# Kernel tuning notes

Hardware: AMD Instinct MI355X
Metric: run time of the kernel (lower is better)

Reference implementation:

```python
import jax, jax.numpy as jnp
import numpy as np

KS = 3

def setup_inputs() -> dict:
    key = jax.random.key(0)
    k1, k2, k3 = jax.random.split(key, 3)
    x = jax.random.normal(k1, (4, 4, 256, 36, 36), dtype=jnp.float32)
    target_filter = jax.random.normal(k2, (1024, 256, KS, KS), dtype=jnp.float32) * 0.05
    # per-sample (b=num_img*num_sq=16) positive scale factors; p_n is scaled by ks/offset
    offset = 1.0 + 2.0 * jax.random.uniform(k3, (16, 2), dtype=jnp.float32)
    return {"x": x, "target_filter": target_filter, "offset": offset}


def _deform_sample(xf, offset, ks):
    # xf: [b, ct, h, w] -> bilinearly sampled x_offset: [b, ct, h, w, N], N = ks*ks
    b, ct, h, w = xf.shape
    N = ks * ks
    pad = ks // 2
    xp = jnp.pad(xf, ((0, 0), (0, 0), (pad, pad), (pad, pad)))  # zero padding as in torch
    Hp, Wp = h + 2 * pad, w + 2 * pad
    dt = xf.dtype
    # kernel grid offsets p_n (row-major: n = i*ks + j, i=row/x, j=col/y)
    r = jnp.arange(-(ks - 1) // 2, (ks - 1) // 2 + 1, dtype=dt)
    pnx, pny = jnp.meshgrid(r, r, indexing='ij')
    pnx = pnx.reshape(N)
    pny = pny.reshape(N)
    # base positions p_0 (in padded coordinates)
    p0x = jnp.arange(pad, h + pad, dtype=dt)
    p0y = jnp.arange(pad, w + pad, dtype=dt)
    # per-sample scales ks / offset
    sx = (ks / offset[:, 0])[:, None, None, None]  # [b,1,1,1]
    sy = (ks / offset[:, 1])[:, None, None, None]
    # sampling positions, kept factored: px [b,h,1,N], py [b,1,w,N]
    px = p0x[None, :, None, None] + pnx[None, None, None, :] * sx
    py = p0y[None, None, :, None] + pny[None, None, None, :] * sy
    pxc = jnp.clip(px, 0.0, Hp - 1)
    pyc = jnp.clip(py, 0.0, Wp - 1)
    # integer corners (detached/int in torch as well)
    qltx = jnp.clip(jnp.floor(px), 0.0, Hp - 1)
    qrbx = jnp.clip(jnp.floor(px) + 1.0, 0.0, Hp - 1)
    qlty = jnp.clip(jnp.floor(py), 0.0, Wp - 1)
    qrby = jnp.clip(jnp.floor(py) + 1.0, 0.0, Wp - 1)
    qltx_i = jax.lax.stop_gradient(qltx).astype(jnp.int32)
    qrbx_i = jax.lax.stop_gradient(qrbx).astype(jnp.int32)
    qlty_i = jax.lax.stop_gradient(qlty).astype(jnp.int32)
    qrby_i = jax.lax.stop_gradient(qrby).astype(jnp.int32)
    # bilinear weights, factored per-axis (broadcast b,h,1,N x b,1,w,N)
    gx_l = 1.0 + (jax.lax.stop_gradient(qltx) - pxc)
    gx_r = 1.0 - (jax.lax.stop_gradient(qrbx) - pxc)
    gy_l = 1.0 + (jax.lax.stop_gradient(qlty) - pyc)
    gy_r = 1.0 - (jax.lax.stop_gradient(qrby) - pyc)
    xflat = xp.reshape(b, ct, Hp * Wp)

    def gather(qx, qy):
        idx = jnp.broadcast_to(qx * Wp + qy, (b, h, w, N)).reshape(b, h * w * N)
        g = jax.vmap(lambda xb, ib: jnp.take(xb, ib, axis=1))(xflat, idx)
        return g.reshape(b, ct, h, w, N)

    x_off = ((gx_l * gy_l)[:, None] * gather(qltx_i, qlty_i)
             + (gx_r * gy_r)[:, None] * gather(qrbx_i, qrby_i)
             + (gx_l * gy_r)[:, None] * gather(qltx_i, qrby_i)
             + (gx_r * gy_l)[:, None] * gather(qrbx_i, qlty_i))
    return x_off  # [b, ct, h, w, N]


def reference(x, target_filter, offset):
    # feat_group=False path of DeformConv2d.forward
    ks = target_filter.shape[-1]
    num_img, num_sq, ct, h, w = x.shape
    xf = x.reshape(num_img * num_sq, ct, h, w)
    x_off = _deform_sample(xf, offset, ks)  # [b, ct, h, w, ks*ks]
    out_ch = target_filter.shape[0]
    outg = out_ch // num_sq
    # grouped conv2d with stride=ks over the im2col-style layout == direct einsum
    f = target_filter.reshape(num_sq, outg, ct, ks, ks)
    xo = x_off.reshape(num_img, num_sq, ct, h, w, ks, ks)
    out = jnp.einsum('gocij,mgcyxij->mgoyx', f, xo)
    return out.reshape(num_img, out_ch, h, w)
```

## Files before the change

### kernel.cpp

```cpp
#include <hip/hip_runtime.h>
#include <hip/hip_bf16.h>


#define HH 36
#define WW 36
#define CT 256
#define NB 16
#define KK 2304
#define NP 1296
#define OCH 1024
#define OUTG 256

typedef __attribute__((ext_vector_type(8))) short short8;
typedef __attribute__((ext_vector_type(4))) float f32x4;
typedef __attribute__((ext_vector_type(4))) unsigned short us4;
typedef __attribute__((ext_vector_type(4))) unsigned uint4v;

__device__ __forceinline__ unsigned short f2bf(float v) {
    unsigned u = __float_as_uint(v);
    u += 0x7fffu + ((u >> 16) & 1u);
    return (unsigned short)(u >> 16);
}
__device__ __forceinline__ unsigned pk2bf(float lo, float hi) {
    __hip_bfloat162 h = __float22bfloat162_rn(float2{lo, hi});
    return *reinterpret_cast<unsigned*>(&h);
}

__global__ __launch_bounds__(256) void cvt_filter(const float* __restrict__ f,
                                                  unsigned short* __restrict__ w) {
    const int o = blockIdx.x;
    const float* fo = f + (size_t)o * KK;
    unsigned short* wo = w + (size_t)o * KK;
    for (int k4 = threadIdx.x * 4; k4 < KK; k4 += 1024) {
        int n = k4 >> 8;
        int c = k4 & 255;
        us4 v;
#pragma unroll
        for (int cc = 0; cc < 4; ++cc) v[cc] = f2bf(fo[(c + cc) * 9 + n]);
        *reinterpret_cast<us4*>(wo + k4) = v;
    }
}

__global__ __launch_bounds__(256) void sample_kernel(const float* __restrict__ x,
                                                     const float* __restrict__ off,
                                                     unsigned short* __restrict__ xt) {
    const int wid = (blockIdx.x & 7) * 144 + (blockIdx.x >> 3);
    const int b = wid / 72;
    const int rem = wid - b * 72;
    const int y = rem >> 1;
    const int half = rem & 1;
    const int tid = threadIdx.x;
    const float sx = 3.0f / off[2 * b + 0];
    const float sy = 3.0f / off[2 * b + 1];

    int qxl[3], qxr[3]; float gxl[3], gxr[3];
    bool lok[3], rok[3];
#pragma unroll
    for (int i = 0; i < 3; ++i) {
        float px = (float)(y + 1) + (float)(i - 1) * sx;
        float pc = fminf(fmaxf(px, 0.f), 37.f);
        float fl = floorf(px);
        float ql = fminf(fmaxf(fl, 0.f), 37.f);
        float qr = fminf(fmaxf(fl + 1.f, 0.f), 37.f);
        qxl[i] = (int)ql; qxr[i] = (int)qr;
        gxl[i] = 1.f + (ql - pc);
        gxr[i] = 1.f - (qr - pc);
        lok[i] = (qxl[i] >= 1 && qxl[i] <= 36);
        rok[i] = (qxr[i] >= 1 && qxr[i] <= 36);
    }

    __shared__ int   s_qyl[HH * 3], s_qyr[HH * 3];
    __shared__ float s_gyl[HH * 3], s_gyr[HH * 3];
    if (tid < HH * 3) {
        int xx = tid / 3, j = tid % 3;
        float py = (float)(xx + 1) + (float)(j - 1) * sy;
        float pc = fminf(fmaxf(py, 0.f), 37.f);
        float fl = floorf(py);
        float ql = fminf(fmaxf(fl, 0.f), 37.f);
        float qr = fminf(fmaxf(fl + 1.f, 0.f), 37.f);
        s_qyl[tid] = (int)ql; s_qyr[tid] = (int)qr;
        s_gyl[tid] = 1.f + (ql - pc);
        s_gyr[tid] = 1.f - (qr - pc);
    }

    __shared__ float xr[3 * 38 * 64];

    for (int chunk = 0; chunk < 2; ++chunk) {
        const int c0 = half * 128 + chunk * 64;
        __syncthreads();

        for (int t = tid; t < 384; t += 256) {
            int i = t / 128, r3 = t & 127;
            int col = (r3 & 64) ? 37 : 0, c = r3 & 63;
            xr[(i * 38 + col) * 64 + c] = 0.f;
        }

        const float* xb = x + (size_t)(b * CT + c0) * NP;
        for (int t = tid; t < 3 * 64 * 9; t += 256) {
            const int i = t / 576;
            const int r2 = t - i * 576;
            const int c = r2 / 9;
            const int cq = r2 - c * 9;
            const int colb = 1 + cq * 4;
            const float* xc = xb + c * NP;
            float4 vl = make_float4(0.f, 0.f, 0.f, 0.f);
            float4 vr = vl;
            if (lok[i]) vl = *(const float4*)(xc + (qxl[i] - 1) * WW + colb - 1);
            if (rok[i]) vr = *(const float4*)(xc + (qxr[i] - 1) * WW + colb - 1);
            float* dst = &xr[(i * 38 + colb) * 64 + c];
            dst[0]   = gxl[i] * vl.x + gxr[i] * vr.x;
            dst[64]  = gxl[i] * vl.y + gxr[i] * vr.y;
            dst[128] = gxl[i] * vl.z + gxr[i] * vr.z;
            dst[192] = gxl[i] * vl.w + gxr[i] * vr.w;
        }
        __syncthreads();

        for (int t = tid; t < 36 * 8; t += 256) {
            const int xi = t >> 3;
            const int c8 = t & 7;
            unsigned short* op = xt + ((size_t)b * NP + y * WW + xi) * KK + c0 + c8 * 8;
#pragma unroll
            for (int n = 0; n < 9; ++n) {
                const int i = n / 3, j = n - i * 3;
                const int tq = xi * 3 + j;
                const float gl = s_gyl[tq], gr = s_gyr[tq];
                const float* L = &xr[(i * 38 + s_qyl[tq]) * 64 + c8 * 8];
                const float* R = &xr[(i * 38 + s_qyr[tq]) * 64 + c8 * 8];
                f32x4 L0 = *(const f32x4*)L, L1 = *(const f32x4*)(L + 4);
                f32x4 R0 = *(const f32x4*)R, R1 = *(const f32x4*)(R + 4);
                uint4v w;
                w[0] = pk2bf(gl * L0[0] + gr * R0[0], gl * L0[1] + gr * R0[1]);
                w[1] = pk2bf(gl * L0[2] + gr * R0[2], gl * L0[3] + gr * R0[3]);
                w[2] = pk2bf(gl * L1[0] + gr * R1[0], gl * L1[1] + gr * R1[1]);
                w[3] = pk2bf(gl * L1[2] + gr * R1[2], gl * L1[3] + gr * R1[3]);
                *reinterpret_cast<uint4v*>(op + n * 256) = w;
            }
        }
    }
}

__global__ __launch_bounds__(256) void gemm_kernel(const unsigned short* __restrict__ wbf,
                                                   const unsigned short* __restrict__ xt,
                                                   float* __restrict__ out) {
    const int wid = (blockIdx.x & 7) * 84 + (blockIdx.x >> 3);
    const int b = wid / 42;
    const int rem = wid - b * 42;
    const int mt = rem / 21;
    const int nt = rem - mt * 21;
    const int m0 = mt * 128;
    const int p0 = nt * 64;
    const int g = b & 3;
    const int mimg = b >> 2;

    const unsigned short* Ab = wbf + (size_t)(g * OUTG + m0) * KK;
    const unsigned short* Bb = xt + (size_t)b * NP * KK;

    __shared__ __align__(16) unsigned short As[2][128 * 64];
    __shared__ __align__(16) unsigned short Bs[2][64 * 64];

    const int tid = threadIdx.x;
    const int wave = tid >> 6, lane = tid & 63;
    const int wr = wave >> 1, wc = wave & 1;
    const int l8 = lane >> 3;
    const int sgrp = (lane & 7) ^ l8;

    f32x4 acc[4][2] = {};

#define STAGE(BUF, KT) do {                                                       \
    const int k0_ = (KT) * 64;                                                    \
    _Pragma("unroll")                                                             \
    for (int ii = 0; ii < 4; ++ii) {                                              \
        const int inst = wave * 4 + ii;                                           \
        const int row = inst * 8 + l8;                                            \
        const unsigned short* srcA = Ab + (size_t)row * KK + k0_ + sgrp * 8;      \
        __builtin_amdgcn_global_load_lds(                                         \
            (const __attribute__((address_space(1))) void*)srcA,                  \
            (__attribute__((address_space(3))) void*)&As[BUF][inst * 512], 16, 0, 0); \
    }                                                                             \
    _Pragma("unroll")                                                             \
    for (int ii = 0; ii < 2; ++ii) {                                              \
        const int inst = wave * 2 + ii;                                           \
        const int row = inst * 8 + l8;                                            \
        int prow = p0 + row;                                                      \
        prow = prow < NP ? prow : NP - 1;                                         \
        const unsigned short* srcB = Bb + (size_t)prow * KK + k0_ + sgrp * 8;     \
        __builtin_amdgcn_global_load_lds(                                         \
            (const __attribute__((address_space(1))) void*)srcB,                  \
            (__attribute__((address_space(3))) void*)&Bs[BUF][inst * 512], 16, 0, 0); \
    }                                                                             \
} while (0)

#define COMPUTE(BUF) do {                                                         \
    _Pragma("unroll")                                                             \
    for (int kk = 0; kk < 2; ++kk) {                                              \
        short8 a[4], bfr[2];                                                      \
        const int g8 = (((kk * 4) + (lane >> 4)) ^ (lane & 7)) << 3;              \
        const int rA = wr * 64 + (lane & 15);                                     \
        const int rB = wc * 32 + (lane & 15);                                     \
        _Pragma("unroll")                                                         \
        for (int m = 0; m < 4; ++m)                                               \
            a[m] = *(const short8*)&As[BUF][(rA + m * 16) * 64 + g8];             \
        _Pragma("unroll")                                                         \
        for (int n = 0; n < 2; ++n)                                               \
            bfr[n] = *(const short8*)&Bs[BUF][(rB + n * 16) * 64 + g8];           \
        _Pragma("unroll")                                                         \
        for (int m = 0; m < 4; ++m)                                               \
            _Pragma("unroll")                                                     \
            for (int n = 0; n < 2; ++n)                                           \
                acc[m][n] = __builtin_amdgcn_mfma_f32_16x16x32_bf16(              \
                    a[m], bfr[n], acc[m][n], 0, 0, 0);                            \
    }                                                                             \
} while (0)

    STAGE(0, 0);

#pragma unroll 1
    for (int kt = 0; kt < 35; ++kt) {
        STAGE((kt + 1) & 1, kt + 1);
        asm volatile("s_waitcnt vmcnt(6)" ::: "memory");
        __builtin_amdgcn_sched_barrier(0);
        __builtin_amdgcn_s_barrier();
        COMPUTE(kt & 1);
        __builtin_amdgcn_s_barrier();
    }
    asm volatile("s_waitcnt vmcnt(0)" ::: "memory");
    __builtin_amdgcn_sched_barrier(0);
    __builtin_amdgcn_s_barrier();
    COMPUTE(35 & 1);

#undef STAGE
#undef COMPUTE

    float* ob = out + ((size_t)mimg * OCH + g * OUTG) * NP;
    const int o0 = m0 + wr * 64 + ((lane >> 4) << 2);
    const int pc = p0 + wc * 32 + (lane & 15);
#pragma unroll
    for (int n = 0; n < 2; ++n) {
        int p = pc + n * 16;
        if (p >= NP) continue;
#pragma unroll
        for (int m = 0; m < 4; ++m) {
#pragma unroll
            for (int r = 0; r < 4; ++r)
                ob[(size_t)(o0 + m * 16 + r) * NP + p] = acc[m][n][r];
        }
    }
}

extern "C" void kernel_launch(void* const* d_in, const int* in_sizes, int n_in,
                              void* d_out, int out_size, void* d_ws, size_t ws_size,
                              hipStream_t stream) {
    const float* x   = (const float*)d_in[0];
    const float* tf  = (const float*)d_in[1];
    const float* off = (const float*)d_in[2];
    float* out = (float*)d_out;

    unsigned short* xt  = (unsigned short*)d_ws;
    unsigned short* wbf = xt + (size_t)NB * NP * KK;

    hipLaunchKernelGGL(cvt_filter, dim3(OCH), dim3(256), 0, stream, tf, wbf);
    hipLaunchKernelGGL(sample_kernel, dim3(NB * HH * 2), dim3(256), 0, stream, x, off, xt);
    hipLaunchKernelGGL(gemm_kernel, dim3(672), dim3(256), 0, stream, wbf, xt, out);
}
```

Baseline: 72.45 us.

## Load GEMM A-operand directly into registers, bypassing LDS staging

```diff
diff --git a/kernel.cpp b/kernel.cpp
--- a/kernel.cpp
+++ b/kernel.cpp
@@ -139,9 +139,9 @@
     }
 }
 
-__global__ __launch_bounds__(256) void gemm_kernel(const unsigned short* __restrict__ wbf,
-                                                   const unsigned short* __restrict__ xt,
-                                                   float* __restrict__ out) {
+__global__ __launch_bounds__(256, 3) void gemm_kernel(const unsigned short* __restrict__ wbf,
+                                                      const unsigned short* __restrict__ xt,
+                                                      float* __restrict__ out) {
     const int wid = (blockIdx.x & 7) * 84 + (blockIdx.x >> 3);
     const int b = wid / 42;
     const int rem = wid - b * 42;
@@ -155,7 +155,6 @@
     const unsigned short* Ab = wbf + (size_t)(g * OUTG + m0) * KK;
     const unsigned short* Bb = xt + (size_t)b * NP * KK;
 
-    __shared__ __align__(16) unsigned short As[2][128 * 64];
     __shared__ __align__(16) unsigned short Bs[2][64 * 64];
 
     const int tid = threadIdx.x;
@@ -164,19 +163,22 @@
     const int l8 = lane >> 3;
     const int sgrp = (lane & 7) ^ l8;
 
+    const unsigned short* Abase = Ab + (size_t)(wr * 64 + (lane & 15)) * KK + ((lane >> 4) * 8);
+
     f32x4 acc[4][2] = {};
-
-#define STAGE(BUF, KT) do {                                                       \
+    short8 aP[8], aN[8];
+
+#define LOADA(DST, KT) do {                                                       \
+    const unsigned short* ab_ = Abase + (KT) * 64;                                \
+    _Pragma("unroll")                                                             \
+    for (int m = 0; m < 4; ++m) {                                                 \
+        DST[m]     = *(const short8*)(ab_ + (size_t)(m * 16) * KK);               \
+        DST[4 + m] = *(const short8*)(ab_ + (size_t)(m * 16) * KK + 32);          \
+    }                                                                             \
+} while (0)
+
+#define STAGE_B(BUF, KT) do {                                                     \
     const int k0_ = (KT) * 64;                                                    \
-    _Pragma("unroll")                                                             \
-    for (int ii = 0; ii < 4; ++ii) {                                              \
-        const int inst = wave * 4 + ii;                                           \
-        const int row = inst * 8 + l8;                                            \
-        const unsigned short* srcA = Ab + (size_t)row * KK + k0_ + sgrp * 8;      \
-        __builtin_amdgcn_global_load_lds(                                         \
-            (const __attribute__((address_space(1))) void*)srcA,                  \
-            (__attribute__((address_space(3))) void*)&As[BUF][inst * 512], 16, 0, 0); \
-    }                                                                             \
     _Pragma("unroll")                                                             \
     for (int ii = 0; ii < 2; ++ii) {                                              \
         const int inst = wave * 2 + ii;                                           \
@@ -190,16 +192,12 @@
     }                                                                             \
 } while (0)
 
-#define COMPUTE(BUF) do {                                                         \
+#define COMPUTE(BUF, AF) do {                                                     \
     _Pragma("unroll")                                                             \
     for (int kk = 0; kk < 2; ++kk) {                                              \
-        short8 a[4], bfr[2];                                                      \
+        short8 bfr[2];                                                            \
         const int g8 = (((kk * 4) + (lane >> 4)) ^ (lane & 7)) << 3;              \
-        const int rA = wr * 64 + (lane & 15);                                     \
         const int rB = wc * 32 + (lane & 15);                                     \
-        _Pragma("unroll")                                                         \
-        for (int m = 0; m < 4; ++m)                                               \
-            a[m] = *(const short8*)&As[BUF][(rA + m * 16) * 64 + g8];             \
         _Pragma("unroll")                                                         \
         for (int n = 0; n < 2; ++n)                                               \
             bfr[n] = *(const short8*)&Bs[BUF][(rB + n * 16) * 64 + g8];           \
@@ -208,27 +206,41 @@
             _Pragma("unroll")                                                     \
             for (int n = 0; n < 2; ++n)                                           \
                 acc[m][n] = __builtin_amdgcn_mfma_f32_16x16x32_bf16(              \
-                    a[m], bfr[n], acc[m][n], 0, 0, 0);                            \
+                    AF[kk * 4 + m], bfr[n], acc[m][n], 0, 0, 0);                  \
     }                                                                             \
 } while (0)
 
-    STAGE(0, 0);
+    LOADA(aP, 0);
+    STAGE_B(0, 0);
 
 #pragma unroll 1
-    for (int kt = 0; kt < 35; ++kt) {
-        STAGE((kt + 1) & 1, kt + 1);
-        asm volatile("s_waitcnt vmcnt(6)" ::: "memory");
+    for (int kt = 0; kt < 34; kt += 2) {
+        LOADA(aN, kt + 1); STAGE_B(1, kt + 1);
+        asm volatile("s_waitcnt vmcnt(10)" ::: "memory");
         __builtin_amdgcn_sched_barrier(0);
         __builtin_amdgcn_s_barrier();
-        COMPUTE(kt & 1);
-        __builtin_amdgcn_s_barrier();
-    }
+        COMPUTE(0, aP);
+        __builtin_amdgcn_s_barrier();
+        LOADA(aP, kt + 2); STAGE_B(0, kt + 2);
+        asm volatile("s_waitcnt vmcnt(10)" ::: "memory");
+        __builtin_amdgcn_sched_barrier(0);
+        __builtin_amdgcn_s_barrier();
+        COMPUTE(1, aN);
+        __builtin_amdgcn_s_barrier();
+    }
+    LOADA(aN, 35); STAGE_B(1, 35);
+    asm volatile("s_waitcnt vmcnt(10)" ::: "memory");
+    __builtin_amdgcn_sched_barrier(0);
+    __builtin_amdgcn_s_barrier();
+    COMPUTE(0, aP);
+    __builtin_amdgcn_s_barrier();
     asm volatile("s_waitcnt vmcnt(0)" ::: "memory");
     __builtin_amdgcn_sched_barrier(0);
     __builtin_amdgcn_s_barrier();
-    COMPUTE(35 & 1);
-
-#undef STAGE
+    COMPUTE(1, aN);
+
+#undef LOADA
+#undef STAGE_B
 #undef COMPUTE
 
     float* ob = out + ((size_t)mimg * OCH + g * OUTG) * NP;
```

New measurement: 144.1 us. 1.99x slower.

## Split K across wave pairs in GEMM with LDS reduction of partial tiles

Applied to the files above, without the earlier changes.

```diff
diff --git a/kernel.cpp b/kernel.cpp
--- a/kernel.cpp
+++ b/kernel.cpp
@@ -160,11 +160,12 @@
 
     const int tid = threadIdx.x;
     const int wave = tid >> 6, lane = tid & 63;
-    const int wr = wave >> 1, wc = wave & 1;
+    const int kkw = wave >> 1;
+    const int wrw = wave & 1;
     const int l8 = lane >> 3;
     const int sgrp = (lane & 7) ^ l8;
 
-    f32x4 acc[4][2] = {};
+    f32x4 acc[4][4] = {};
 
 #define STAGE(BUF, KT) do {                                                       \
     const int k0_ = (KT) * 64;                                                    \
@@ -191,25 +192,22 @@
 } while (0)
 
 #define COMPUTE(BUF) do {                                                         \
-    _Pragma("unroll")                                                             \
-    for (int kk = 0; kk < 2; ++kk) {                                              \
-        short8 a[4], bfr[2];                                                      \
-        const int g8 = (((kk * 4) + (lane >> 4)) ^ (lane & 7)) << 3;              \
-        const int rA = wr * 64 + (lane & 15);                                     \
-        const int rB = wc * 32 + (lane & 15);                                     \
+    short8 a[4], bfr[4];                                                          \
+    const int g8 = (((kkw * 4) + (lane >> 4)) ^ (lane & 7)) << 3;                 \
+    const int rA = wrw * 64 + (lane & 15);                                        \
+    const int rB = (lane & 15);                                                   \
+    _Pragma("unroll")                                                             \
+    for (int m = 0; m < 4; ++m)                                                   \
+        a[m] = *(const short8*)&As[BUF][(rA + m * 16) * 64 + g8];                 \
+    _Pragma("unroll")                                                             \
+    for (int n = 0; n < 4; ++n)                                                   \
+        bfr[n] = *(const short8*)&Bs[BUF][(rB + n * 16) * 64 + g8];               \
+    _Pragma("unroll")                                                             \
+    for (int m = 0; m < 4; ++m)                                                   \
         _Pragma("unroll")                                                         \
-        for (int m = 0; m < 4; ++m)                                               \
-            a[m] = *(const short8*)&As[BUF][(rA + m * 16) * 64 + g8];             \
-        _Pragma("unroll")                                                         \
-        for (int n = 0; n < 2; ++n)                                               \
-            bfr[n] = *(const short8*)&Bs[BUF][(rB + n * 16) * 64 + g8];           \
-        _Pragma("unroll")                                                         \
-        for (int m = 0; m < 4; ++m)                                               \
-            _Pragma("unroll")                                                     \
-            for (int n = 0; n < 2; ++n)                                           \
-                acc[m][n] = __builtin_amdgcn_mfma_f32_16x16x32_bf16(              \
-                    a[m], bfr[n], acc[m][n], 0, 0, 0);                            \
-    }                                                                             \
+        for (int n = 0; n < 4; ++n)                                               \
+            acc[m][n] = __builtin_amdgcn_mfma_f32_16x16x32_bf16(                  \
+                a[m], bfr[n], acc[m][n], 0, 0, 0);                                \
 } while (0)
 
     STAGE(0, 0);
@@ -231,18 +229,39 @@
 #undef STAGE
 #undef COMPUTE
 
-    float* ob = out + ((size_t)mimg * OCH + g * OUTG) * NP;
-    const int o0 = m0 + wr * 64 + ((lane >> 4) << 2);
-    const int pc = p0 + wc * 32 + (lane & 15);
-#pragma unroll
-    for (int n = 0; n < 2; ++n) {
-        int p = pc + n * 16;
-        if (p >= NP) continue;
-#pragma unroll
-        for (int m = 0; m < 4; ++m) {
-#pragma unroll
-            for (int r = 0; r < 4; ++r)
-                ob[(size_t)(o0 + m * 16 + r) * NP + p] = acc[m][n][r];
+    __syncthreads();
+    float* red = reinterpret_cast<float*>(&As[0][0]);
+    if (wave >= 2) {
+#pragma unroll
+        for (int m = 0; m < 4; ++m)
+#pragma unroll
+            for (int n = 0; n < 4; ++n)
+                *reinterpret_cast<f32x4*>(
+                    &red[(size_t)wrw * 4096 + (m * 4 + n) * 256 + lane * 4]) = acc[m][n];
+    }
+    __syncthreads();
+    if (wave < 2) {
+#pragma unroll
+        for (int m = 0; m < 4; ++m)
+#pragma unroll
+            for (int n = 0; n < 4; ++n) {
+                f32x4 p = *reinterpret_cast<const f32x4*>(
+                    &red[(size_t)wrw * 4096 + (m * 4 + n) * 256 + lane * 4]);
+                acc[m][n] += p;
+            }
+        float* ob = out + ((size_t)mimg * OCH + g * OUTG) * NP;
+        const int o0 = m0 + wrw * 64 + ((lane >> 4) << 2);
+        const int pc = p0 + (lane & 15);
+#pragma unroll
+        for (int n = 0; n < 4; ++n) {
+            int p = pc + n * 16;
+            if (p >= NP) continue;
+#pragma unroll
+            for (int m = 0; m < 4; ++m) {
+#pragma unroll
+                for (int r = 0; r < 4; ++r)
+                    ob[(size_t)(o0 + m * 16 + r) * NP + p] = acc[m][n][r];
+            }
         }
     }
 }
```

New measurement: 96.78 us. 1.34x slower.

## Load B operand directly from global into registers, bypassing LDS

Applied to the files above, without the earlier changes.

```diff
diff --git a/kernel.cpp b/kernel.cpp
--- a/kernel.cpp
+++ b/kernel.cpp
@@ -156,7 +156,6 @@
     const unsigned short* Bb = xt + (size_t)b * NP * KK;
 
     __shared__ __align__(16) unsigned short As[2][128 * 64];
-    __shared__ __align__(16) unsigned short Bs[2][64 * 64];
 
     const int tid = threadIdx.x;
     const int wave = tid >> 6, lane = tid & 63;
@@ -164,9 +163,15 @@
     const int l8 = lane >> 3;
     const int sgrp = (lane & 7) ^ l8;
 
+    const int brow0 = min(p0 + wc * 32 + (lane & 15),      NP - 1);
+    const int brow1 = min(p0 + wc * 32 + (lane & 15) + 16, NP - 1);
+    const unsigned short* Bbase0 = Bb + (size_t)brow0 * KK + ((lane >> 4) * 8);
+    const unsigned short* Bbase1 = Bb + (size_t)brow1 * KK + ((lane >> 4) * 8);
+
     f32x4 acc[4][2] = {};
-
-#define STAGE(BUF, KT) do {                                                       \
+    short8 bP0, bP1, bP2, bP3, bN0, bN1, bN2, bN3;
+
+#define STAGE_A(BUF, KT) do {                                                     \
     const int k0_ = (KT) * 64;                                                    \
     _Pragma("unroll")                                                             \
     for (int ii = 0; ii < 4; ++ii) {                                              \
@@ -177,58 +182,74 @@
             (const __attribute__((address_space(1))) void*)srcA,                  \
             (__attribute__((address_space(3))) void*)&As[BUF][inst * 512], 16, 0, 0); \
     }                                                                             \
-    _Pragma("unroll")                                                             \
-    for (int ii = 0; ii < 2; ++ii) {                                              \
-        const int inst = wave * 2 + ii;                                           \
-        const int row = inst * 8 + l8;                                            \
-        int prow = p0 + row;                                                      \
-        prow = prow < NP ? prow : NP - 1;                                         \
-        const unsigned short* srcB = Bb + (size_t)prow * KK + k0_ + sgrp * 8;     \
-        __builtin_amdgcn_global_load_lds(                                         \
-            (const __attribute__((address_space(1))) void*)srcB,                  \
-            (__attribute__((address_space(3))) void*)&Bs[BUF][inst * 512], 16, 0, 0); \
+} while (0)
+
+#define LOADB(KT, B0, B1, B2, B3) do {                                            \
+    const int kb_ = (KT) * 64;                                                    \
+    B0 = *(const short8*)(Bbase0 + kb_);                                          \
+    B1 = *(const short8*)(Bbase0 + kb_ + 32);                                     \
+    B2 = *(const short8*)(Bbase1 + kb_);                                          \
+    B3 = *(const short8*)(Bbase1 + kb_ + 32);                                     \
+    asm volatile("" : "+v"(B0), "+v"(B1), "+v"(B2), "+v"(B3));                    \
+} while (0)
+
+#define COMPUTE(BUF, B0, B1, B2, B3) do {                                         \
+    short8 a[4];                                                                  \
+    const int rA = wr * 64 + (lane & 15);                                         \
+    {   const int g8 = ((lane >> 4) ^ (lane & 7)) << 3;                           \
+        _Pragma("unroll")                                                         \
+        for (int m = 0; m < 4; ++m)                                               \
+            a[m] = *(const short8*)&As[BUF][(rA + m * 16) * 64 + g8];             \
+        _Pragma("unroll")                                                         \
+        for (int m = 0; m < 4; ++m) {                                             \
+            acc[m][0] = __builtin_amdgcn_mfma_f32_16x16x32_bf16(a[m], B0, acc[m][0], 0, 0, 0); \
+            acc[m][1] = __builtin_amdgcn_mfma_f32_16x16x32_bf16(a[m], B2, acc[m][1], 0, 0, 0); \
+        }                                                                         \
+    }                                                                             \
+    {   const int g8 = ((4 + (lane >> 4)) ^ (lane & 7)) << 3;                     \
+        _Pragma("unroll")                                                         \
+        for (int m = 0; m < 4; ++m)                                               \
+            a[m] = *(const short8*)&As[BUF][(rA + m * 16) * 64 + g8];             \
+        _Pragma("unroll")                                                         \
+        for (int m = 0; m < 4; ++m) {                                             \
+            acc[m][0] = __builtin_amdgcn_mfma_f32_16x16x32_bf16(a[m], B1, acc[m][0], 0, 0, 0); \
+            acc[m][1] = __builtin_amdgcn_mfma_f32_16x16x32_bf16(a[m], B3, acc[m][1], 0, 0, 0); \
+        }                                                                         \
     }                                                                             \
 } while (0)
 
-#define COMPUTE(BUF) do {                                                         \
-    _Pragma("unroll")                                                             \
-    for (int kk = 0; kk < 2; ++kk) {                                              \
-        short8 a[4], bfr[2];                                                      \
-        const int g8 = (((kk * 4) + (lane >> 4)) ^ (lane & 7)) << 3;              \
-        const int rA = wr * 64 + (lane & 15);                                     \
-        const int rB = wc * 32 + (lane & 15);                                     \
-        _Pragma("unroll")                                                         \
-        for (int m = 0; m < 4; ++m)                                               \
-            a[m] = *(const short8*)&As[BUF][(rA + m * 16) * 64 + g8];             \
-        _Pragma("unroll")                                                         \
-        for (int n = 0; n < 2; ++n)                                               \
-            bfr[n] = *(const short8*)&Bs[BUF][(rB + n * 16) * 64 + g8];           \
-        _Pragma("unroll")                                                         \
-        for (int m = 0; m < 4; ++m)                                               \
-            _Pragma("unroll")                                                     \
-            for (int n = 0; n < 2; ++n)                                           \
-                acc[m][n] = __builtin_amdgcn_mfma_f32_16x16x32_bf16(              \
-                    a[m], bfr[n], acc[m][n], 0, 0, 0);                            \
-    }                                                                             \
-} while (0)
-
-    STAGE(0, 0);
-
-#pragma unroll 1
-    for (int kt = 0; kt < 35; ++kt) {
-        STAGE((kt + 1) & 1, kt + 1);
-        asm volatile("s_waitcnt vmcnt(6)" ::: "memory");
-        __builtin_amdgcn_sched_barrier(0);
-        __builtin_amdgcn_s_barrier();
-        COMPUTE(kt & 1);
-        __builtin_amdgcn_s_barrier();
-    }
+    STAGE_A(0, 0);
+    LOADB(0, bP0, bP1, bP2, bP3);
     asm volatile("s_waitcnt vmcnt(0)" ::: "memory");
     __builtin_amdgcn_sched_barrier(0);
     __builtin_amdgcn_s_barrier();
-    COMPUTE(35 & 1);
-
-#undef STAGE
+
+#pragma unroll 1
+    for (int kt = 0; kt < 34; kt += 2) {
+        STAGE_A(1, kt + 1);
+        LOADB(kt + 1, bN0, bN1, bN2, bN3);
+        COMPUTE(0, bP0, bP1, bP2, bP3);
+        asm volatile("s_waitcnt vmcnt(0)" ::: "memory");
+        __builtin_amdgcn_sched_barrier(0);
+        __builtin_amdgcn_s_barrier();
+
+        STAGE_A(0, kt + 2);
+        LOADB(kt + 2, bP0, bP1, bP2, bP3);
+        COMPUTE(1, bN0, bN1, bN2, bN3);
+        asm volatile("s_waitcnt vmcnt(0)" ::: "memory");
+        __builtin_amdgcn_sched_barrier(0);
+        __builtin_amdgcn_s_barrier();
+    }
+    STAGE_A(1, 35);
+    LOADB(35, bN0, bN1, bN2, bN3);
+    COMPUTE(0, bP0, bP1, bP2, bP3);
+    asm volatile("s_waitcnt vmcnt(0)" ::: "memory");
+    __builtin_amdgcn_sched_barrier(0);
+    __builtin_amdgcn_s_barrier();
+    COMPUTE(1, bN0, bN1, bN2, bN3);
+
+#undef STAGE_A
+#undef LOADB
 #undef COMPUTE
 
     float* ob = out + ((size_t)mimg * OCH + g * OUTG) * NP;
```

Measured after the change: 111.3 us. 53.6% more time.
